# Kernel optimization log

Measured on AMD Instinct MI355X. Metric: run time of the kernel, lower is better.

Reference implementation:

```python
import jax, jax.numpy as jnp
import numpy as np

NUM_USR = 100000
NUM_ENT = 1000000
NUM_REL = 32
DIM = 32
K = 16          # neighbor_sample_size
N_ITER = 2
B = 4096


def setup_inputs() -> dict:
    key = jax.random.key(0)
    ks = jax.random.split(key, 9)
    u = jax.random.randint(ks[0], (B,), 0, NUM_USR, dtype=jnp.int32)
    v = jax.random.randint(ks[1], (B,), 0, NUM_ENT, dtype=jnp.int32)
    adj_ent = jax.random.randint(ks[2], (NUM_ENT, K), 0, NUM_ENT, dtype=jnp.int32)
    adj_rel = jax.random.randint(ks[3], (NUM_ENT, K), 0, NUM_REL, dtype=jnp.int32)
    # xavier-normal-ish embedding tables and Linear(dim, dim)
    usr_w = jax.random.normal(ks[4], (NUM_USR, DIM), dtype=jnp.float32) * 0.02
    ent_w = jax.random.normal(ks[5], (NUM_ENT, DIM), dtype=jnp.float32) * 0.02
    rel_w = jax.random.normal(ks[6], (NUM_REL, DIM), dtype=jnp.float32) * 0.02
    W = jax.random.normal(ks[7], (DIM, DIM), dtype=jnp.float32) * (1.0 / np.sqrt(DIM))
    b = jnp.zeros((DIM,), dtype=jnp.float32)
    return {"u": u, "v": v, "usr_w": usr_w, "ent_w": ent_w, "rel_w": rel_w,
            "W": W, "b": b, "adj_ent": adj_ent, "adj_rel": adj_rel}


def _kgcn_forward(u, v, usr_w, ent_w, rel_w, W, b, adj_ent, adj_rel):
    user = usr_w[u]                                # [B, D]
    # hop expansion: entities [B,1] -> [B,K] -> [B,K^2]
    ents = [v.reshape(B, 1)]
    rels = []
    for h in range(N_ITER):
        ents.append(adj_ent[ents[h]].reshape(B, -1))
        rels.append(adj_rel[ents[h]].reshape(B, -1))
    ev = [ent_w[e] for e in ents]                  # [B, K^h, D]
    rv = [rel_w[r] for r in rels]
    for i in range(N_ITER):
        act = jnp.tanh if i == N_ITER - 1 else jax.nn.sigmoid
        nxt = []
        for hop in range(N_ITER - i):
            sv = ev[hop]                                    # [B, n, D]
            nv = ev[hop + 1].reshape(B, -1, K, DIM)         # [B, n, K, D]
            nr = rv[hop].reshape(B, -1, K, DIM)             # [B, n, K, D]
            scores = jnp.einsum('bd,bnkd->bnk', user, nr)   # user-relation attention
            attn = jax.nn.softmax(scores, axis=-1)          # over K neighbors
            agg = jnp.einsum('bnk,bnkd->bnd', attn, nv)
            out = (sv + agg) @ W.T + b                      # 'sum' aggregator Linear
            nxt.append(act(out))
        ev = nxt
    item = ev[0].reshape(B, DIM)
    return jax.nn.sigmoid(jnp.sum(user * item, axis=1))    # [B]


def reference(u, v, usr_w, ent_w, rel_w, W, b, adj_ent, adj_rel):
    return _kgcn_forward(u, v, usr_w, ent_w, rel_w, W, b, adj_ent, adj_rel)
```

## Files before the change

### kernel.cpp

```cpp
#include <hip/hip_runtime.h>
#include <math.h>

#define BATCH 4096
#define DIM   32
#define KNB   16
#define PAD   33


__global__ __launch_bounds__(256) void kgcn_kernel(
    const int*   __restrict__ u,
    const int*   __restrict__ v,
    const float* __restrict__ usr_w,
    const float* __restrict__ ent_w,
    const float* __restrict__ rel_w,
    const float* __restrict__ W,
    const float* __restrict__ bvec,
    const int*   __restrict__ adj_ent,
    const int*   __restrict__ adj_rel,
    float*       __restrict__ out)
{
    __shared__ float relw_s[DIM * PAD];
    __shared__ float Ws[DIM * PAD];
    __shared__ float b_s[DIM];
    __shared__ float user_s[DIM];
    __shared__ float e0_s[DIM];
    __shared__ int   ent1_s[KNB], rel1_s[KNB];
    __shared__ int   ent2_s[KNB * KNB], rel2_s[KNB * KNB];
    __shared__ float e1_s[KNB * PAD];
    __shared__ float sc2_s[KNB * 17];
    __shared__ float attn2_s[KNB * 17];
    __shared__ float sc1_s[KNB];
    __shared__ float attn1_s[KNB];
    __shared__ float tmp_s[KNB * PAD];
    __shared__ float h1_s[KNB * PAD];
    __shared__ float tmp0_s[DIM];
    __shared__ float h0_s[DIM];

    const int t  = threadIdx.x;
    const int bb = blockIdx.x;

    #pragma unroll
    for (int i = 0; i < 4; ++i) {
        int idx = t + i * 256;
        int r = idx >> 5, d = idx & 31;
        relw_s[r * PAD + d] = rel_w[idx];
        Ws[r * PAD + d]     = W[idx];
    }
    const int vid = v[bb];
    if (t < 32) {
        user_s[t] = usr_w[(size_t)u[bb] * DIM + t];
        if (t == 0) { }
    } else if (t < 64) {
        e0_s[t - 32] = ent_w[(size_t)vid * DIM + (t - 32)];
    } else if (t < 80) {
        ent1_s[t - 64] = adj_ent[(size_t)vid * KNB + (t - 64)];
    } else if (t < 96) {
        rel1_s[t - 80] = adj_rel[(size_t)vid * KNB + (t - 80)];
    } else if (t < 128) {
        b_s[t - 96] = bvec[t - 96];
    }
    __syncthreads();

    {
        int parent = ent1_s[t >> 4];
        ent2_s[t] = adj_ent[(size_t)parent * KNB + (t & 15)];
        rel2_s[t] = adj_rel[(size_t)parent * KNB + (t & 15)];
    }
    #pragma unroll
    for (int i = 0; i < 2; ++i) {
        int idx = t + i * 256;
        int n = idx >> 5, d = idx & 31;
        e1_s[n * PAD + d] = ent_w[(size_t)ent1_s[n] * DIM + d];
    }
    __syncthreads();

    {
        int r = rel2_s[t];
        float s = 0.f;
        #pragma unroll
        for (int d = 0; d < DIM; ++d) s += user_s[d] * relw_s[r * PAD + d];
        sc2_s[(t >> 4) * 17 + (t & 15)] = s;
    }
    if (t < KNB) {
        int r = rel1_s[t];
        float s = 0.f;
        #pragma unroll
        for (int d = 0; d < DIM; ++d) s += user_s[d] * relw_s[r * PAD + d];
        sc1_s[t] = s;
    }
    __syncthreads();

    {
        int n = t >> 4;
        float mx = -1e30f;
        #pragma unroll
        for (int k = 0; k < KNB; ++k) mx = fmaxf(mx, sc2_s[n * 17 + k]);
        float sum = 0.f;
        #pragma unroll
        for (int k = 0; k < KNB; ++k) sum += expf(sc2_s[n * 17 + k] - mx);
        attn2_s[n * 17 + (t & 15)] = expf(sc2_s[n * 17 + (t & 15)] - mx) / sum;
    }
    if (t < KNB) {
        float mx = -1e30f;
        #pragma unroll
        for (int k = 0; k < KNB; ++k) mx = fmaxf(mx, sc1_s[k]);
        float sum = 0.f;
        #pragma unroll
        for (int k = 0; k < KNB; ++k) sum += expf(sc1_s[k] - mx);
        attn1_s[t] = expf(sc1_s[t] - mx) / sum;
    }
    __syncthreads();

    #pragma unroll
    for (int ro = 0; ro < 2; ++ro) {
        int n = (t >> 5) + ro * 8;
        int d = t & 31;
        float agg = 0.f;
        #pragma unroll
        for (int k = 0; k < KNB; ++k) {
            agg += attn2_s[n * 17 + k] *
                   ent_w[(size_t)ent2_s[n * KNB + k] * DIM + d];
        }
        tmp_s[n * PAD + d] = e1_s[n * PAD + d] + agg;
    }
    __syncthreads();
    #pragma unroll
    for (int ro = 0; ro < 2; ++ro) {
        int n = (t >> 5) + ro * 8;
        int o = t & 31;
        float h = b_s[o];
        #pragma unroll
        for (int d = 0; d < DIM; ++d) h += tmp_s[n * PAD + d] * Ws[o * PAD + d];
        h1_s[n * PAD + o] = 1.f / (1.f + expf(-h));
    }
    __syncthreads();

    if (t < 32) {
        float agg = 0.f;
        #pragma unroll
        for (int k = 0; k < KNB; ++k) agg += attn1_s[k] * e1_s[k * PAD + t];
        tmp0_s[t] = e0_s[t] + agg;
    }
    __syncthreads();
    if (t < 32) {
        float h = b_s[t];
        #pragma unroll
        for (int d = 0; d < DIM; ++d) h += tmp0_s[d] * Ws[t * PAD + d];
        h0_s[t] = 1.f / (1.f + expf(-h));
    }
    __syncthreads();

    if (t < 32) {
        float agg = 0.f;
        #pragma unroll
        for (int k = 0; k < KNB; ++k) agg += attn1_s[k] * h1_s[k * PAD + t];
        tmp0_s[t] = h0_s[t] + agg;
    }
    __syncthreads();
    if (t < 32) {
        float h = b_s[t];
        #pragma unroll
        for (int d = 0; d < DIM; ++d) h += tmp0_s[d] * Ws[t * PAD + d];
        float item = tanhf(h);
        float p = user_s[t] * item;
        #pragma unroll
        for (int off = 16; off; off >>= 1) p += __shfl_down(p, off, 32);
        if (t == 0) out[bb] = 1.f / (1.f + expf(-p));
    }
}

extern "C" void kernel_launch(void* const* d_in, const int* in_sizes, int n_in,
                              void* d_out, int out_size, void* d_ws, size_t ws_size,
                              hipStream_t stream) {
    const int*   u       = (const int*)d_in[0];
    const int*   v       = (const int*)d_in[1];
    const float* usr_w   = (const float*)d_in[2];
    const float* ent_w   = (const float*)d_in[3];
    const float* rel_w   = (const float*)d_in[4];
    const float* W       = (const float*)d_in[5];
    const float* bvec    = (const float*)d_in[6];
    const int*   adj_ent = (const int*)d_in[7];
    const int*   adj_rel = (const int*)d_in[8];
    float* out = (float*)d_out;

    kgcn_kernel<<<BATCH, 256, 0, stream>>>(u, v, usr_w, ent_w, rel_w, W, bvec,
                                           adj_ent, adj_rel, out);
}
```

Baseline: 260.2 us.

## Precompute relation scores, prefetch neighbor embeddings as float2, shuffle-based softmax

Computes the 32 user-relation scores once instead of one 32-wide dot product per neighbor, and drops the shared rel_w copy. The 16 hop-2 neighbor embeddings are loaded as float2 into registers before the softmax, so those gathers overlap with the attention computation. The softmax now uses cross-lane shuffles with fast exp, and several small stages are merged to remove barriers. It also adds a 4-blocks occupancy hint and switches to 32-bit index math, which assumes offsets fit in int and adds register pressure from the 16-entry buffer.

```diff
diff --git a/kernel.cpp b/kernel.cpp
--- a/kernel.cpp
+++ b/kernel.cpp
@@ -4,10 +4,11 @@
 #define BATCH 4096
 #define DIM   32
 #define KNB   16
-#define PAD   33
+#define PADW  33
+#define PADV  34
 
 
-__global__ __launch_bounds__(256) void kgcn_kernel(
+__global__ __launch_bounds__(256, 4) void kgcn_kernel(
     const int*   __restrict__ u,
     const int*   __restrict__ v,
     const float* __restrict__ usr_w,
@@ -19,153 +20,140 @@
     const int*   __restrict__ adj_rel,
     float*       __restrict__ out)
 {
-    __shared__ float relw_s[DIM * PAD];
-    __shared__ float Ws[DIM * PAD];
-    __shared__ float b_s[DIM];
-    __shared__ float user_s[DIM];
-    __shared__ float e0_s[DIM];
+    __shared__ float Ws[DIM * PADW];
+    __shared__ float user_s[DIM], e0_s[DIM], b_s[DIM], sc_s[DIM];
     __shared__ int   ent1_s[KNB], rel1_s[KNB];
-    __shared__ int   ent2_s[KNB * KNB], rel2_s[KNB * KNB];
-    __shared__ float e1_s[KNB * PAD];
-    __shared__ float sc2_s[KNB * 17];
+    __shared__ int   eoff2_s[KNB * KNB];
+    __shared__ float e1_s[KNB * PADV];
     __shared__ float attn2_s[KNB * 17];
-    __shared__ float sc1_s[KNB];
     __shared__ float attn1_s[KNB];
-    __shared__ float tmp_s[KNB * PAD];
-    __shared__ float h1_s[KNB * PAD];
+    __shared__ float tmp_s[KNB * PADV];
+    __shared__ float h1_s[KNB * PADV];
     __shared__ float tmp0_s[DIM];
-    __shared__ float h0_s[DIM];
 
     const int t  = threadIdx.x;
     const int bb = blockIdx.x;
+    const int vid = v[bb];
 
     #pragma unroll
     for (int i = 0; i < 4; ++i) {
         int idx = t + i * 256;
-        int r = idx >> 5, d = idx & 31;
-        relw_s[r * PAD + d] = rel_w[idx];
-        Ws[r * PAD + d]     = W[idx];
+        Ws[(idx >> 5) * PADW + (idx & 31)] = W[idx];
     }
-    const int vid = v[bb];
     if (t < 32) {
-        user_s[t] = usr_w[(size_t)u[bb] * DIM + t];
-        if (t == 0) { }
+        user_s[t] = usr_w[u[bb] * DIM + t];
     } else if (t < 64) {
-        e0_s[t - 32] = ent_w[(size_t)vid * DIM + (t - 32)];
+        e0_s[t - 32] = ent_w[vid * DIM + (t - 32)];
     } else if (t < 80) {
-        ent1_s[t - 64] = adj_ent[(size_t)vid * KNB + (t - 64)];
+        ent1_s[t - 64] = adj_ent[vid * KNB + (t - 64)];
     } else if (t < 96) {
-        rel1_s[t - 80] = adj_rel[(size_t)vid * KNB + (t - 80)];
+        rel1_s[t - 80] = adj_rel[vid * KNB + (t - 80)];
     } else if (t < 128) {
         b_s[t - 96] = bvec[t - 96];
     }
     __syncthreads();
 
+    int rel2;
     {
         int parent = ent1_s[t >> 4];
-        ent2_s[t] = adj_ent[(size_t)parent * KNB + (t & 15)];
-        rel2_s[t] = adj_rel[(size_t)parent * KNB + (t & 15)];
+        rel2       = adj_rel[parent * KNB + (t & 15)];
+        eoff2_s[t] = adj_ent[parent * KNB + (t & 15)] * DIM;
     }
+    if (t < 32) {
+        const float* rw = rel_w + t * DIM;
+        float s = 0.f;
+        #pragma unroll
+        for (int d = 0; d < DIM; ++d) s += user_s[d] * rw[d];
+        sc_s[t] = s;
+    }
+    __syncthreads();
+
+    const int n  = t >> 4;
+    const int d2 = t & 15;
+    const float2* ew2 = (const float2*)ent_w;
+
+    float2 vbuf[KNB];
     #pragma unroll
-    for (int i = 0; i < 2; ++i) {
-        int idx = t + i * 256;
-        int n = idx >> 5, d = idx & 31;
-        e1_s[n * PAD + d] = ent_w[(size_t)ent1_s[n] * DIM + d];
+    for (int k = 0; k < KNB; ++k)
+        vbuf[k] = ew2[(eoff2_s[n * KNB + k] >> 1) + d2];
+    float2 ev = ew2[ent1_s[n] * (DIM / 2) + d2];
+    *(float2*)&e1_s[n * PADV + 2 * d2] = ev;
+
+    {
+        float s2 = sc_s[rel2];
+        float m = s2;
+        #pragma unroll
+        for (int msk = 1; msk < 16; msk <<= 1) m = fmaxf(m, __shfl_xor(m, msk, 16));
+        float p = __expf(s2 - m);
+        float q = p;
+        #pragma unroll
+        for (int msk = 1; msk < 16; msk <<= 1) q += __shfl_xor(q, msk, 16);
+        attn2_s[n * 17 + d2] = p / q;
+    }
+    if (t < KNB) {
+        float s1 = sc_s[rel1_s[t]];
+        float m = s1;
+        #pragma unroll
+        for (int msk = 1; msk < 16; msk <<= 1) m = fmaxf(m, __shfl_xor(m, msk, 16));
+        float p = __expf(s1 - m);
+        float q = p;
+        #pragma unroll
+        for (int msk = 1; msk < 16; msk <<= 1) q += __shfl_xor(q, msk, 16);
+        attn1_s[t] = p / q;
     }
     __syncthreads();
 
     {
-        int r = rel2_s[t];
-        float s = 0.f;
+        float2 a = make_float2(0.f, 0.f);
         #pragma unroll
-        for (int d = 0; d < DIM; ++d) s += user_s[d] * relw_s[r * PAD + d];
-        sc2_s[(t >> 4) * 17 + (t & 15)] = s;
-    }
-    if (t < KNB) {
-        int r = rel1_s[t];
-        float s = 0.f;
-        #pragma unroll
-        for (int d = 0; d < DIM; ++d) s += user_s[d] * relw_s[r * PAD + d];
-        sc1_s[t] = s;
-    }
-    __syncthreads();
-
-    {
-        int n = t >> 4;
-        float mx = -1e30f;
-        #pragma unroll
-        for (int k = 0; k < KNB; ++k) mx = fmaxf(mx, sc2_s[n * 17 + k]);
-        float sum = 0.f;
-        #pragma unroll
-        for (int k = 0; k < KNB; ++k) sum += expf(sc2_s[n * 17 + k] - mx);
-        attn2_s[n * 17 + (t & 15)] = expf(sc2_s[n * 17 + (t & 15)] - mx) / sum;
-    }
-    if (t < KNB) {
-        float mx = -1e30f;
-        #pragma unroll
-        for (int k = 0; k < KNB; ++k) mx = fmaxf(mx, sc1_s[k]);
-        float sum = 0.f;
-        #pragma unroll
-        for (int k = 0; k < KNB; ++k) sum += expf(sc1_s[k] - mx);
-        attn1_s[t] = expf(sc1_s[t] - mx) / sum;
+        for (int k = 0; k < KNB; ++k) {
+            float w = attn2_s[n * 17 + k];
+            a.x += w * vbuf[k].x;
+            a.y += w * vbuf[k].y;
+        }
+        float2 tv = make_float2(ev.x + a.x, ev.y + a.y);
+        *(float2*)&tmp_s[n * PADV + 2 * d2] = tv;
     }
     __syncthreads();
 
     #pragma unroll
     for (int ro = 0; ro < 2; ++ro) {
-        int n = (t >> 5) + ro * 8;
-        int d = t & 31;
-        float agg = 0.f;
-        #pragma unroll
-        for (int k = 0; k < KNB; ++k) {
-            agg += attn2_s[n * 17 + k] *
-                   ent_w[(size_t)ent2_s[n * KNB + k] * DIM + d];
-        }
-        tmp_s[n * PAD + d] = e1_s[n * PAD + d] + agg;
-    }
-    __syncthreads();
-    #pragma unroll
-    for (int ro = 0; ro < 2; ++ro) {
-        int n = (t >> 5) + ro * 8;
-        int o = t & 31;
+        int nn = (t >> 5) + 8 * ro;
+        int o  = t & 31;
         float h = b_s[o];
         #pragma unroll
-        for (int d = 0; d < DIM; ++d) h += tmp_s[n * PAD + d] * Ws[o * PAD + d];
-        h1_s[n * PAD + o] = 1.f / (1.f + expf(-h));
+        for (int d = 0; d < DIM; ++d) h += tmp_s[nn * PADV + d] * Ws[o * PADW + d];
+        h1_s[nn * PADV + o] = 1.f / (1.f + __expf(-h));
+    }
+    if (t < 32) {
+        float a0 = 0.f;
+        #pragma unroll
+        for (int k = 0; k < KNB; ++k) a0 += attn1_s[k] * e1_s[k * PADV + t];
+        tmp0_s[t] = e0_s[t] + a0;
     }
     __syncthreads();
 
     if (t < 32) {
-        float agg = 0.f;
-        #pragma unroll
-        for (int k = 0; k < KNB; ++k) agg += attn1_s[k] * e1_s[k * PAD + t];
-        tmp0_s[t] = e0_s[t] + agg;
-    }
-    __syncthreads();
-    if (t < 32) {
         float h = b_s[t];
         #pragma unroll
-        for (int d = 0; d < DIM; ++d) h += tmp0_s[d] * Ws[t * PAD + d];
-        h0_s[t] = 1.f / (1.f + expf(-h));
+        for (int d = 0; d < DIM; ++d) h += tmp0_s[d] * Ws[t * PADW + d];
+        float h0 = 1.f / (1.f + __expf(-h));
+        float a1 = 0.f;
+        #pragma unroll
+        for (int k = 0; k < KNB; ++k) a1 += attn1_s[k] * h1_s[k * PADV + t];
+        tmp0_s[t] = h0 + a1;
     }
     __syncthreads();
 
     if (t < 32) {
-        float agg = 0.f;
-        #pragma unroll
-        for (int k = 0; k < KNB; ++k) agg += attn1_s[k] * h1_s[k * PAD + t];
-        tmp0_s[t] = h0_s[t] + agg;
-    }
-    __syncthreads();
-    if (t < 32) {
         float h = b_s[t];
         #pragma unroll
-        for (int d = 0; d < DIM; ++d) h += tmp0_s[d] * Ws[t * PAD + d];
+        for (int d = 0; d < DIM; ++d) h += tmp0_s[d] * Ws[t * PADW + d];
         float item = tanhf(h);
         float p = user_s[t] * item;
         #pragma unroll
         for (int off = 16; off; off >>= 1) p += __shfl_down(p, off, 32);
-        if (t == 0) out[bb] = 1.f / (1.f + expf(-p));
+        if (t == 0) out[bb] = 1.f / (1.f + __expf(-p));
     }
 }
 
```

New measurement: 259.2 us. About the same (-0.4%).
